# Optimization experiments

Hardware: AMD Instinct MI355X
Metric: run time of the kernel (lower is better)

The kernel has to match this reference:

```python
import jax, jax.numpy as jnp
import numpy as np

CHUNK = 1024  # query points processed per slab to avoid the full [N,M] matrix


def _nn_one(a, b):
    """Nearest-neighbor squared distance + index from each point in a [N,3] to set b [M,3]."""
    b_sq = jnp.sum(b * b, axis=-1)  # [M]

    def chunk_fn(ac):  # ac: [CHUNK, 3]
        # squared euclidean distance slab [CHUNK, M]
        d = jnp.sum(ac * ac, axis=-1)[:, None] + b_sq[None, :] - 2.0 * (ac @ b.T)
        return jnp.min(d, axis=-1), jnp.argmin(d, axis=-1).astype(jnp.int32)

    n = a.shape[0]
    a_chunks = a.reshape(n // CHUNK, CHUNK, 3)
    dmin, idx = jax.lax.map(chunk_fn, a_chunks)
    return dmin.reshape(n), idx.reshape(n)


def setup_inputs() -> dict:
    key = jax.random.key(0)
    k1, k2 = jax.random.split(key)
    B, N, M = 2, 16384, 16384
    xyz1 = jax.random.normal(k1, (B, N, 3), dtype=jnp.float32)
    xyz2 = jax.random.normal(k2, (B, M, 3), dtype=jnp.float32)
    return {"xyz1": xyz1, "xyz2": xyz2}


def reference(xyz1, xyz2):
    # ChamferDistanceFunction.forward with return_idx=True
    dist1, idx1 = jax.vmap(_nn_one)(xyz1, xyz2)  # [B,N], [B,N]
    dist2, idx2 = jax.vmap(_nn_one)(xyz2, xyz1)  # [B,M], [B,M]
    return dist1, dist2, idx1, idx2
```

## Files before the change

kernel.cpp:

```cpp
#include <hip/hip_runtime.h>

#define NPTS 16384
#define GRID 16
#define SGRID 8
#define NCELL 4096
#define CS_STRIDE (NCELL+1)
#define GLO -4.0f
#define GH 0.5f
#define GINVH 2.0f


__device__ __forceinline__ int clamp16(int v){ return v<0?0:(v>15?15:v); }
__device__ __forceinline__ int spr3(int v){
    return (v&1) | ((v&2)<<2) | ((v&4)<<4) | ((v&8)<<6);
}
__device__ __forceinline__ int mcode(int ix,int iy,int iz){
    return spr3(ix) | (spr3(iy)<<1) | (spr3(iz)<<2);
}

__global__ __launch_bounds__(256) void zero_hist(int* __restrict__ hist){
    hist[blockIdx.x*256 + threadIdx.x] = 0;
}

__global__ __launch_bounds__(256) void bin_kernel(
    const float* __restrict__ xyz1, const float* __restrict__ xyz2,
    int* __restrict__ hist)
{
    int t = blockIdx.x*256 + threadIdx.x;
    int s = t >> 14, i = t & (NPTS-1);
    const float* src = (s < 2 ? xyz1 : xyz2) + ((size_t)(s&1)*NPTS + i)*3;
    float x = src[0], y = src[1], z = src[2];
    int ix = clamp16((int)floorf((x-GLO)*GINVH));
    int iy = clamp16((int)floorf((y-GLO)*GINVH));
    int iz = clamp16((int)floorf((z-GLO)*GINVH));
    atomicAdd(&hist[s*NCELL + mcode(ix,iy,iz)], 1);
}

__global__ __launch_bounds__(1024) void scan_kernel(
    const int* __restrict__ hist, int* __restrict__ cellStart, int* __restrict__ cursor)
{
    int s = blockIdx.x, tid = threadIdx.x, lane = tid & 63, w = tid >> 6;
    const int* h = hist + s*NCELL;
    int v0 = h[tid*4+0], v1 = h[tid*4+1], v2 = h[tid*4+2], v3 = h[tid*4+3];
    int tsum = v0+v1+v2+v3;
    int x = tsum;
    #pragma unroll
    for (int d = 1; d < 64; d <<= 1) { int y = __shfl_up(x, d, 64); if (lane >= d) x += y; }
    __shared__ int wsum[16];
    if (lane == 63) wsum[w] = x;
    __syncthreads();
    if (tid == 0) { int acc = 0; for (int i2 = 0; i2 < 16; ++i2) { int tt = wsum[i2]; wsum[i2] = acc; acc += tt; } }
    __syncthreads();
    int excl = x - tsum + wsum[w];
    int* cs = cellStart + s*CS_STRIDE;
    int* cu = cursor   + s*NCELL;
    cs[tid*4+0] = excl; cu[tid*4+0] = excl; excl += v0;
    cs[tid*4+1] = excl; cu[tid*4+1] = excl; excl += v1;
    cs[tid*4+2] = excl; cu[tid*4+2] = excl; excl += v2;
    cs[tid*4+3] = excl; cu[tid*4+3] = excl; excl += v3;
    if (tid == 1023) cs[NCELL] = excl;
}

__global__ __launch_bounds__(256) void scatter_kernel(
    const float* __restrict__ xyz1, const float* __restrict__ xyz2,
    int* __restrict__ cursor, float4* __restrict__ spts)
{
    int t = blockIdx.x*256 + threadIdx.x;
    int s = t >> 14, i = t & (NPTS-1);
    const float* src = (s < 2 ? xyz1 : xyz2) + ((size_t)(s&1)*NPTS + i)*3;
    float x = src[0], y = src[1], z = src[2];
    int ix = clamp16((int)floorf((x-GLO)*GINVH));
    int iy = clamp16((int)floorf((y-GLO)*GINVH));
    int iz = clamp16((int)floorf((z-GLO)*GINVH));
    int code = mcode(ix,iy,iz);
    int pos = atomicAdd(&cursor[s*NCELL + code], 1);
    spts[s*NPTS + pos] = make_float4(x, y, z, __int_as_float(i));
}

__global__ __launch_bounds__(256) void nn_kernel(
    const float4* __restrict__ spts,
    const int* __restrict__ cellStart, float* __restrict__ out)
{
    const int gt   = blockIdx.x*256 + threadIdx.x;
    const int lane = gt & 63;
    const int wv   = gt >> 6;
    const int set  = wv >> 11;
    const int dir  = set >> 1;
    const int b    = set & 1;
    const int qset = (dir == 0) ? b : 2 + b;
    const int cset = (dir == 0) ? 2 + b : b;
    const int qbase = (wv & 2047) << 3;
    const int qsub  = lane >> 3;
    const int sub   = lane & 7;
    const int qpos  = qbase + qsub;

    float4 q = spts[qset*NPTS + qpos];
    const int qorig = __float_as_int(q.w);
    const float ax = q.x, ay = q.y, az = q.z;
    const float aw = __fadd_rn(__fadd_rn(__fmul_rn(ax,ax), __fmul_rn(ay,ay)), __fmul_rn(az,az));

    int ix = clamp16((int)floorf((ax-GLO)*GINVH));
    int iy = clamp16((int)floorf((ay-GLO)*GINVH));
    int iz = clamp16((int)floorf((az-GLO)*GINVH));

    int bx0 = ix, bx1 = ix, by0 = iy, by1 = iy, bz0 = iz, bz1 = iz;
    #pragma unroll
    for (int m = 32; m; m >>= 1) {
        bx0 = min(bx0, __shfl_xor(bx0, m, 64)); bx1 = max(bx1, __shfl_xor(bx1, m, 64));
        by0 = min(by0, __shfl_xor(by0, m, 64)); by1 = max(by1, __shfl_xor(by1, m, 64));
        bz0 = min(bz0, __shfl_xor(bz0, m, 64)); bz1 = max(bz1, __shfl_xor(bz1, m, 64));
    }
    const int sx0 = __builtin_amdgcn_readfirstlane(bx0 >> 1);
    const int sx1 = __builtin_amdgcn_readfirstlane(bx1 >> 1);
    const int sy0 = __builtin_amdgcn_readfirstlane(by0 >> 1);
    const int sy1 = __builtin_amdgcn_readfirstlane(by1 >> 1);
    const int sz0 = __builtin_amdgcn_readfirstlane(bz0 >> 1);
    const int sz1 = __builtin_amdgcn_readfirstlane(bz1 >> 1);

    const float4* cp = spts + cset*NPTS;
    const int*    cs = cellStart + cset*CS_STRIDE;

    float bd = __builtin_inff(); int bi = 0;

    #define EVAL(c4)                                                             \
    {                                                                            \
        float bsq = __fadd_rn(__fadd_rn(__fmul_rn((c4).x,(c4).x),                \
                                        __fmul_rn((c4).y,(c4).y)),               \
                              __fmul_rn((c4).z,(c4).z));                         \
        float tt = fmaf(az, (c4).z, fmaf(ay, (c4).y, __fmul_rn(ax, (c4).x)));    \
        float dd = fmaf(-2.0f, tt, __fadd_rn(aw, bsq));                          \
        int cix = __float_as_int((c4).w);                                        \
        bool bet = (dd < bd) || (dd == bd && cix < bi);                          \
        bd = bet ? dd : bd; bi = bet ? cix : bi;                                 \
    }

    #define SCAN_RANGE(j0, j1)                                                   \
    {                                                                            \
        int j = (j0) + sub;                                                      \
        for (; j + 24 < (j1); j += 32) {                                         \
            float4 c0 = cp[j];                                                   \
            float4 c1 = cp[j+8];                                                 \
            float4 c2 = cp[j+16];                                                \
            float4 c3 = cp[j+24];                                                \
            EVAL(c0); EVAL(c1); EVAL(c2); EVAL(c3);                              \
        }                                                                        \
        for (; j < (j1); j += 8) {                                               \
            float4 c4 = cp[j];                                                   \
            EVAL(c4);                                                            \
        }                                                                        \
    }

    {
        int s0 = qbase + 4 - 80; if (s0 < 0) s0 = 0;
        int e0 = s0 + 160;       if (e0 > NPTS) { e0 = NPTS; s0 = e0 - 160; }
        s0 = __builtin_amdgcn_readfirstlane(s0);
        e0 = __builtin_amdgcn_readfirstlane(e0);
        SCAN_RANGE(s0, e0);
    }

    for (int s = 0; s <= 8; ++s) {
        int zlo = max(0, sz0 - s), zhi = min(SGRID-1, sz1 + s);
        int ylo = max(0, sy0 - s), yhi = min(SGRID-1, sy1 + s);
        int xlo = max(0, sx0 - s), xhi = min(SGRID-1, sx1 + s);
        for (int scz = zlo; scz <= zhi; ++scz) {
            int cdz = max(0, max(sz0 - scz, scz - sz1));
            float lo = (scz == 0)       ? -1e30f : (GLO + (float)(scz*2    )*GH);
            float hi = (scz == SGRID-1) ?  1e30f : (GLO + (float)(scz*2 + 2)*GH);
            float dzz = fmaxf(0.0f, fmaxf(lo - az, az - hi));
            float dz2 = __fmul_rn(dzz, dzz);
            for (int scy = ylo; scy <= yhi; ++scy) {
                int cdy = max(cdz, max(0, max(sy0 - scy, scy - sy1)));
                if (cdy > s) continue;
                lo = (scy == 0)       ? -1e30f : (GLO + (float)(scy*2    )*GH);
                hi = (scy == SGRID-1) ?  1e30f : (GLO + (float)(scy*2 + 2)*GH);
                float dyy = fmaxf(0.0f, fmaxf(lo - ay, ay - hi));
                float dyz2 = fmaf(dyy, dyy, dz2);
                int sbyz = (spr3(scy)<<1) | (spr3(scz)<<2);
                for (int scx = xlo; scx <= xhi; ++scx) {
                    int cd = max(cdy, max(0, max(sx0 - scx, scx - sx1)));
                    if (cd != s) continue;
                    lo = (scx == 0)       ? -1e30f : (GLO + (float)(scx*2    )*GH);
                    hi = (scx == SGRID-1) ?  1e30f : (GLO + (float)(scx*2 + 2)*GH);
                    float dxx = fmaxf(0.0f, fmaxf(lo - ax, ax - hi));
                    float lb = fmaf(dxx, dxx, dyz2);
                    if (__ballot(fmaf(0.995f, lb, -3e-4f) <= bd) == 0ULL) continue;
                    int sb = spr3(scx) | sbyz;
                    int j0 = __builtin_amdgcn_readfirstlane(cs[sb<<3]);
                    int j1 = __builtin_amdgcn_readfirstlane(cs[(sb+1)<<3]);
                    SCAN_RANGE(j0, j1);
                }
            }
        }
        float wmax = bd;
        #pragma unroll
        for (int m = 32; m; m >>= 1) wmax = fmaxf(wmax, __shfl_xor(wmax, m, 64));
        float rs = (float)s;
        if (fmaf(0.995f, rs*rs, -3e-4f) > wmax) break;
        if (xlo == 0 && ylo == 0 && zlo == 0 &&
            xhi == SGRID-1 && yhi == SGRID-1 && zhi == SGRID-1) break;
    }

    #undef SCAN_RANGE
    #undef EVAL

    #pragma unroll
    for (int m = 1; m < 8; m <<= 1) {
        float od = __shfl_xor(bd, m, 64);
        int   oi = __shfl_xor(bi, m, 64);
        bool bet = (od < bd) || (od == bd && oi < bi);
        bd = bet ? od : bd; bi = bet ? oi : bi;
    }

    if (sub == 0) {
        int off  = dir ? 32768 : 0;
        int slot = b*NPTS + qorig;
        out[off + slot]         = bd;
        out[65536 + off + slot] = (float)bi;
    }
}

__global__ __launch_bounds__(256) void nn_full(
    const float* __restrict__ xyz1, const float* __restrict__ xyz2,
    float* __restrict__ out)
{
    int qid = blockIdx.x*256 + threadIdx.x;
    int dir = qid >> 15;
    int q15 = qid & 32767;
    const float* qsrc = dir ? xyz2 : xyz1;
    float ax = qsrc[q15*3+0], ay = qsrc[q15*3+1], az = qsrc[q15*3+2];
    float asq = __fadd_rn(__fadd_rn(__fmul_rn(ax,ax), __fmul_rn(ay,ay)), __fmul_rn(az,az));
    const float* cp = (dir ? xyz1 : xyz2) + (size_t)(q15 & NPTS)*3;
    float bd = 3.402823466e+38f; int bi = 0;
    for (int j = 0; j < NPTS; ++j) {
        float bx = cp[3*j+0], by = cp[3*j+1], bz = cp[3*j+2];
        float bsq = __fadd_rn(__fadd_rn(__fmul_rn(bx,bx), __fmul_rn(by,by)), __fmul_rn(bz,bz));
        float tt = fmaf(az, bz, fmaf(ay, by, __fmul_rn(ax, bx)));
        float d = fmaf(-2.0f, tt, __fadd_rn(asq, bsq));
        if (d < bd) { bd = d; bi = j; }
    }
    int off = dir ? 32768 : 0;
    out[off + q15]         = bd;
    out[65536 + off + q15] = (float)bi;
}

extern "C" void kernel_launch(void* const* d_in, const int* in_sizes, int n_in,
                              void* d_out, int out_size, void* d_ws, size_t ws_size,
                              hipStream_t stream) {
    const float* xyz1 = (const float*)d_in[0];
    const float* xyz2 = (const float*)d_in[1];
    float* out = (float*)d_out;

    const size_t off_spts = 0;
    const size_t off_cs   = 1048576;
    const size_t off_hist = 1114128;
    const size_t off_cur  = 1179664;
    const size_t need     = 1245200;

    if (d_ws != nullptr && ws_size >= need) {
        float4* spts = (float4*)((char*)d_ws + off_spts);
        int* cstart  = (int*)((char*)d_ws + off_cs);
        int* hist    = (int*)((char*)d_ws + off_hist);
        int* cursor  = (int*)((char*)d_ws + off_cur);
        zero_hist   <<<64,  256, 0, stream>>>(hist);
        bin_kernel  <<<256, 256, 0, stream>>>(xyz1, xyz2, hist);
        scan_kernel <<<4,  1024, 0, stream>>>(hist, cstart, cursor);
        scatter_kernel<<<256,256,0, stream>>>(xyz1, xyz2, cursor, spts);
        nn_kernel   <<<2048, 256, 0, stream>>>(spts, cstart, out);
    } else {
        nn_full<<<65536/256, 256, 0, stream>>>(xyz1, xyz2, out);
    }
}
```

Before: 180.2 us.

## Schedule NN waves heaviest-first via density-bucketed permutation

Adds three small kernels that estimate each query group's work from the candidate point count in its super-cell, bucket the groups by that estimate, and build a permutation. The nn_kernel then reads its group index from this permutation so dense, expensive waves are dispatched first. The aim is to reduce tail imbalance from long-running waves. It costs three extra kernel launches and one extra indirection load per wave.

After: 294.2 us. +63.2%, slower.

```diff
diff --git a/kernel.cpp b/kernel.cpp
--- a/kernel.cpp
+++ b/kernel.cpp
@@ -8,6 +8,7 @@
 #define GLO -4.0f
 #define GH 0.5f
 #define GINVH 2.0f
+#define NOCT 8192
 
 
 __device__ __forceinline__ int clamp16(int v){ return v<0?0:(v>15?15:v); }
@@ -18,8 +19,11 @@
     return spr3(ix) | (spr3(iy)<<1) | (spr3(iz)<<2);
 }
 
-__global__ __launch_bounds__(256) void zero_hist(int* __restrict__ hist){
+__global__ __launch_bounds__(256) void zero_hist(int* __restrict__ hist,
+                                                 int* __restrict__ bcnt,
+                                                 int* __restrict__ bcur){
     hist[blockIdx.x*256 + threadIdx.x] = 0;
+    if (blockIdx.x == 0 && threadIdx.x < 32) { bcnt[threadIdx.x] = 0; bcur[threadIdx.x] = 0; }
 }
 
 __global__ __launch_bounds__(256) void bin_kernel(
@@ -77,13 +81,53 @@
     spts[s*NPTS + pos] = make_float4(x, y, z, __int_as_float(i));
 }
 
+__global__ __launch_bounds__(256) void sched_weight(
+    const float4* __restrict__ spts, const int* __restrict__ cellStart,
+    int* __restrict__ octbkt, int* __restrict__ bcnt)
+{
+    int o = blockIdx.x*256 + threadIdx.x;
+    int set = o >> 11, dir = set >> 1, b = set & 1;
+    int qset = (dir == 0) ? b : 2 + b;
+    int cset = (dir == 0) ? 2 + b : b;
+    int qbase = (o & 2047) << 3;
+    float4 q = spts[qset*NPTS + qbase + 4];
+    int sx = clamp16((int)floorf((q.x-GLO)*GINVH)) >> 1;
+    int sy = clamp16((int)floorf((q.y-GLO)*GINVH)) >> 1;
+    int sz = clamp16((int)floorf((q.z-GLO)*GINVH)) >> 1;
+    int sb = spr3(sx) | (spr3(sy)<<1) | (spr3(sz)<<2);
+    const int* cs = cellStart + cset*CS_STRIDE;
+    int cnt = cs[(sb+1)<<3] - cs[sb<<3];
+    int bkt = 31 - min(31, cnt >> 5);
+    octbkt[o] = bkt;
+    atomicAdd(&bcnt[bkt], 1);
+}
+
+__global__ __launch_bounds__(64) void sched_scan(
+    const int* __restrict__ bcnt, int* __restrict__ bcur)
+{
+    if (threadIdx.x == 0) {
+        int acc = 0;
+        for (int k = 0; k < 32; ++k) { bcur[k] = acc; acc += bcnt[k]; }
+    }
+}
+
+__global__ __launch_bounds__(256) void sched_scatter(
+    const int* __restrict__ octbkt, int* __restrict__ bcur, int* __restrict__ perm)
+{
+    int o = blockIdx.x*256 + threadIdx.x;
+    int pos = atomicAdd(&bcur[octbkt[o]], 1);
+    perm[pos] = o;
+}
+
 __global__ __launch_bounds__(256) void nn_kernel(
     const float4* __restrict__ spts,
-    const int* __restrict__ cellStart, float* __restrict__ out)
+    const int* __restrict__ cellStart, const int* __restrict__ perm,
+    float* __restrict__ out)
 {
     const int gt   = blockIdx.x*256 + threadIdx.x;
     const int lane = gt & 63;
-    const int wv   = gt >> 6;
+    const int slot = gt >> 6;
+    const int wv   = __builtin_amdgcn_readfirstlane(perm[slot]);
     const int set  = wv >> 11;
     const int dir  = set >> 1;
     const int b    = set & 1;
@@ -213,9 +257,9 @@
 
     if (sub == 0) {
         int off  = dir ? 32768 : 0;
-        int slot = b*NPTS + qorig;
-        out[off + slot]         = bd;
-        out[65536 + off + slot] = (float)bi;
+        int slot2 = b*NPTS + qorig;
+        out[off + slot2]         = bd;
+        out[65536 + off + slot2] = (float)bi;
     }
 }
 
@@ -254,18 +298,29 @@
     const size_t off_cs   = 1048576;
     const size_t off_hist = 1114128;
     const size_t off_cur  = 1179664;
-    const size_t need     = 1245200;
+    const size_t off_bkt  = 1245200;
+    const size_t off_bcnt = 1277968;
+    const size_t off_bcur = 1278096;
+    const size_t off_perm = 1278224;
+    const size_t need     = 1310992;
 
     if (d_ws != nullptr && ws_size >= need) {
         float4* spts = (float4*)((char*)d_ws + off_spts);
         int* cstart  = (int*)((char*)d_ws + off_cs);
         int* hist    = (int*)((char*)d_ws + off_hist);
         int* cursor  = (int*)((char*)d_ws + off_cur);
-        zero_hist   <<<64,  256, 0, stream>>>(hist);
-        bin_kernel  <<<256, 256, 0, stream>>>(xyz1, xyz2, hist);
-        scan_kernel <<<4,  1024, 0, stream>>>(hist, cstart, cursor);
-        scatter_kernel<<<256,256,0, stream>>>(xyz1, xyz2, cursor, spts);
-        nn_kernel   <<<2048, 256, 0, stream>>>(spts, cstart, out);
+        int* octbkt  = (int*)((char*)d_ws + off_bkt);
+        int* bcnt    = (int*)((char*)d_ws + off_bcnt);
+        int* bcur    = (int*)((char*)d_ws + off_bcur);
+        int* perm    = (int*)((char*)d_ws + off_perm);
+        zero_hist    <<<64,  256, 0, stream>>>(hist, bcnt, bcur);
+        bin_kernel   <<<256, 256, 0, stream>>>(xyz1, xyz2, hist);
+        scan_kernel  <<<4,  1024, 0, stream>>>(hist, cstart, cursor);
+        scatter_kernel<<<256,256, 0, stream>>>(xyz1, xyz2, cursor, spts);
+        sched_weight <<<32,  256, 0, stream>>>(spts, cstart, octbkt, bcnt);
+        sched_scan   <<<1,    64, 0, stream>>>(bcnt, bcur);
+        sched_scatter<<<32,  256, 0, stream>>>(octbkt, bcur, perm);
+        nn_kernel    <<<2048,256, 0, stream>>>(spts, cstart, perm, out);
     } else {
         nn_full<<<65536/256, 256, 0, stream>>>(xyz1, xyz2, out);
     }
```

## Split candidate scan across two wavefronts per query group and merge partials

Applied to the files above, without the earlier changes.

Each group of 8 query points is now served by two wavefronts, each scanning every other 8-candidate stripe (stride 16), which doubles the grid to 4096 blocks. Partial minima and indices go to a workspace buffer, and a new merge kernel picks the better of the two with index tie-breaking. The aim is more parallelism and shorter per-wave scan loops in the tail-heavy NN search. The cost is duplicated query setup and bounding-box reductions, an extra kernel launch, extra global traffic for the partial results, and a larger workspace requirement.

Result: slower. 193.1 us (+7.2%).

```diff
diff --git a/kernel.cpp b/kernel.cpp
--- a/kernel.cpp
+++ b/kernel.cpp
@@ -8,6 +8,7 @@
 #define GLO -4.0f
 #define GH 0.5f
 #define GINVH 2.0f
+#define NQTOT 65536
 
 
 __device__ __forceinline__ int clamp16(int v){ return v<0?0:(v>15?15:v); }
@@ -79,11 +80,14 @@
 
 __global__ __launch_bounds__(256) void nn_kernel(
     const float4* __restrict__ spts,
-    const int* __restrict__ cellStart, float* __restrict__ out)
+    const int* __restrict__ cellStart,
+    float* __restrict__ pd, int* __restrict__ pi)
 {
     const int gt   = blockIdx.x*256 + threadIdx.x;
     const int lane = gt & 63;
-    const int wv   = gt >> 6;
+    const int slot = gt >> 6;
+    const int wv   = slot >> 1;
+    const int half = slot & 1;
     const int set  = wv >> 11;
     const int dir  = set >> 1;
     const int b    = set & 1;
@@ -92,6 +96,7 @@
     const int qbase = (wv & 2047) << 3;
     const int qsub  = lane >> 3;
     const int sub   = lane & 7;
+    const int csplit = sub + (half << 3);
     const int qpos  = qbase + qsub;
 
     float4 q = spts[qset*NPTS + qpos];
@@ -136,15 +141,15 @@
 
     #define SCAN_RANGE(j0, j1)                                                   \
     {                                                                            \
-        int j = (j0) + sub;                                                      \
-        for (; j + 24 < (j1); j += 32) {                                         \
+        int j = (j0) + csplit;                                                   \
+        for (; j + 48 < (j1); j += 64) {                                         \
             float4 c0 = cp[j];                                                   \
-            float4 c1 = cp[j+8];                                                 \
-            float4 c2 = cp[j+16];                                                \
-            float4 c3 = cp[j+24];                                                \
+            float4 c1 = cp[j+16];                                                \
+            float4 c2 = cp[j+32];                                                \
+            float4 c3 = cp[j+48];                                                \
             EVAL(c0); EVAL(c1); EVAL(c2); EVAL(c3);                              \
         }                                                                        \
-        for (; j < (j1); j += 8) {                                               \
+        for (; j < (j1); j += 16) {                                              \
             float4 c4 = cp[j];                                                   \
             EVAL(c4);                                                            \
         }                                                                        \
@@ -212,11 +217,24 @@
     }
 
     if (sub == 0) {
-        int off  = dir ? 32768 : 0;
-        int slot = b*NPTS + qorig;
-        out[off + slot]         = bd;
-        out[65536 + off + slot] = (float)bi;
-    }
+        int qid = (dir << 15) + b*NPTS + qorig;
+        pd[half*NQTOT + qid] = bd;
+        pi[half*NQTOT + qid] = bi;
+    }
+}
+
+__global__ __launch_bounds__(256) void merge_kernel(
+    const float* __restrict__ pd, const int* __restrict__ pi,
+    float* __restrict__ out)
+{
+    int qid = blockIdx.x*256 + threadIdx.x;
+    float d0 = pd[qid];          int i0 = pi[qid];
+    float d1 = pd[NQTOT + qid];  int i1 = pi[NQTOT + qid];
+    bool bet = (d1 < d0) || (d1 == d0 && i1 < i0);
+    float bd = bet ? d1 : d0;
+    int   bi = bet ? i1 : i0;
+    out[qid]         = bd;
+    out[NQTOT + qid] = (float)bi;
 }
 
 __global__ __launch_bounds__(256) void nn_full(
@@ -254,18 +272,23 @@
     const size_t off_cs   = 1048576;
     const size_t off_hist = 1114128;
     const size_t off_cur  = 1179664;
-    const size_t need     = 1245200;
+    const size_t off_pd   = 1245200;
+    const size_t off_pi   = 1769488;
+    const size_t need     = 2293776;
 
     if (d_ws != nullptr && ws_size >= need) {
         float4* spts = (float4*)((char*)d_ws + off_spts);
         int* cstart  = (int*)((char*)d_ws + off_cs);
         int* hist    = (int*)((char*)d_ws + off_hist);
         int* cursor  = (int*)((char*)d_ws + off_cur);
+        float* pd    = (float*)((char*)d_ws + off_pd);
+        int*   pi    = (int*)((char*)d_ws + off_pi);
         zero_hist   <<<64,  256, 0, stream>>>(hist);
         bin_kernel  <<<256, 256, 0, stream>>>(xyz1, xyz2, hist);
         scan_kernel <<<4,  1024, 0, stream>>>(hist, cstart, cursor);
         scatter_kernel<<<256,256,0, stream>>>(xyz1, xyz2, cursor, spts);
-        nn_kernel   <<<2048, 256, 0, stream>>>(spts, cstart, out);
+        nn_kernel   <<<4096, 256, 0, stream>>>(spts, cstart, pd, pi);
+        merge_kernel<<<256,  256, 0, stream>>>(pd, pi, out);
     } else {
         nn_full<<<65536/256, 256, 0, stream>>>(xyz1, xyz2, out);
     }
```
